# Optimization experiments

Hardware: AMD Instinct MI355X
Metric: run time of the kernel (lower is better)

Reference implementation:

```python
import jax, jax.numpy as jnp
import numpy as np

EMB = 1024
HEADS = 16
HEAD_DIM = EMB // HEADS


def setup_inputs() -> dict:
    key = jax.random.key(0)
    ks = jax.random.split(key, 6)
    B, S = 4, 1024
    inputs = jax.random.normal(ks[0], (B, S, EMB), dtype=jnp.float32)
    # causal mask: 1.0 where attention is disallowed (added * -1e9 in the layer)
    mask = (1.0 - jnp.tril(jnp.ones((S, S), dtype=jnp.float32)))[None, None, :, :]
    scale = 1.0 / np.sqrt(EMB)
    wq = jax.random.normal(ks[1], (EMB, EMB), dtype=jnp.float32) * scale
    wk = jax.random.normal(ks[2], (EMB, EMB), dtype=jnp.float32) * scale
    wv = jax.random.normal(ks[3], (EMB, EMB), dtype=jnp.float32) * scale
    wo = jax.random.normal(ks[4], (EMB, EMB), dtype=jnp.float32) * scale
    zb = jnp.zeros((EMB,), dtype=jnp.float32)
    return {"inputs": inputs, "mask": mask, "wq": wq, "bq": zb, "wk": wk,
            "bk": zb, "wv": wv, "bv": zb, "wo": wo, "bo": zb}


def _split_heads(t, B):
    # [B, S, E] -> [B, H, S, Dh]
    return t.reshape(B, -1, HEADS, HEAD_DIM).transpose(0, 2, 1, 3)


def reference(inputs, mask, wq, bq, wk, bk, wv, bv, wo, bo):
    B = inputs.shape[0]
    q = _split_heads(inputs @ wq + bq, B)
    k = _split_heads(inputs @ wk + bk, B)
    v = _split_heads(inputs @ wv + bv, B)
    # NOTE: source divides by sqrt(sqrt(head_num)) = head_num**0.25
    scores = jnp.einsum('bhsd,bhtd->bhst', q, k) / jnp.asarray(HEADS, inputs.dtype) ** 0.25
    if mask is not None:
        scores = scores + mask * -1e9
    attn = jax.nn.softmax(scores, axis=-1)
    z = jnp.einsum('bhst,bhtd->bhsd', attn, v)
    # Faithful to source: reshape [B,H,S,Dh] -> [B,S,E] WITHOUT transposing heads back
    z = z.reshape(B, -1, EMB)
    return z @ wo + bo
```

## Files before the change

kernel.cpp:

```cpp
#include <hip/hip_runtime.h>
#include <hip/hip_bf16.h>
#include <stdint.h>

typedef __attribute__((ext_vector_type(8))) short short8;
typedef __attribute__((ext_vector_type(4))) float float4v;

#define SEQ   1024
#define NQKV  3072

__device__ __forceinline__ float bf2f(ushort h) {
    union { uint u; float f; } c; c.u = ((uint)h) << 16; return c.f;
}
__device__ __forceinline__ ushort f2bf(float f) {
    union { uint u; float f; } c; c.f = f;
    uint u = c.u;
    return (ushort)((u + 0x7fffu + ((u >> 16) & 1u)) >> 16);
}
__device__ __forceinline__ void gl2lds16(const ushort* g, ushort* l) {
    __builtin_amdgcn_global_load_lds(
        (const __attribute__((address_space(1))) unsigned int*)(g),
        (__attribute__((address_space(3))) unsigned int*)(l),
        16, 0, 0);
}

__global__ void detect_k(const uint* __restrict__ x, int* __restrict__ flag) {
    __shared__ int cnt[256];
    int h = 0;
    for (int i = threadIdx.x; i < 4096; i += 256) {
        uint w = x[i];
        uint e = (w >> 7) & 0xFFu;
        h += (e >= 100u && e <= 130u) ? 1 : 0;
    }
    cnt[threadIdx.x] = h;
    __syncthreads();
    if (threadIdx.x == 0) {
        int s = 0;
        for (int i = 0; i < 256; i++) s += cnt[i];
        flag[0] = (s > 2048) ? 0 : 1;
    }
}

__global__ __launch_bounds__(256) void xcvt_k(const void* __restrict__ x,
                                              ushort* __restrict__ xc,
                                              const int* __restrict__ flag) {
    if (!*flag) return;
    int i = (blockIdx.x * 256 + threadIdx.x) * 4;
    const float* xf = (const float*)x;
    float4 v = *(const float4*)(xf + i);
    ushort4 o;
    o.x = f2bf(v.x); o.y = f2bf(v.y); o.z = f2bf(v.z); o.w = f2bf(v.w);
    *(ushort4*)(xc + i) = o;
}

__global__ void biascat_k(const void* __restrict__ bq, const void* __restrict__ bk,
                          const void* __restrict__ bv, const void* __restrict__ bo,
                          const int* __restrict__ flag, ushort* __restrict__ bout) {
    int i = blockIdx.x * 256 + threadIdx.x;
    int sel = i >> 10, j = i & 1023;
    const void* p = (sel == 0) ? bq : (sel == 1) ? bk : (sel == 2) ? bv : bo;
    bout[i] = (*flag) ? f2bf(((const float*)p)[j]) : ((const ushort*)p)[j];
}

__global__ __launch_bounds__(256) void transpose4_k(const void* __restrict__ w0,
                                                    const void* __restrict__ w1,
                                                    const void* __restrict__ w2,
                                                    const void* __restrict__ w3,
                                                    ushort* __restrict__ outall,
                                                    const int* __restrict__ flag) {
    __shared__ ushort tile[64][72];
    int z = blockIdx.z;
    const void* in = (z == 0) ? w0 : (z == 1) ? w1 : (z == 2) ? w2 : w3;
    ushort* out = outall + (size_t)z * 1024 * 1024;
    int k0 = blockIdx.x * 64;
    int n0 = blockIdx.y * 64;
    int t = threadIdx.x;
    int r = t >> 3, c = (t & 7) * 8;
    bool isf = (*flag != 0);
#pragma unroll
    for (int p = 0; p < 2; p++) {
        int rr = r + p * 32;
        if (isf) {
            const float* src = (const float*)in + (size_t)(k0 + rr) * 1024 + n0 + c;
            float4 v0 = *(const float4*)src;
            float4 v1 = *(const float4*)(src + 4);
            tile[rr][c + 0] = f2bf(v0.x); tile[rr][c + 1] = f2bf(v0.y);
            tile[rr][c + 2] = f2bf(v0.z); tile[rr][c + 3] = f2bf(v0.w);
            tile[rr][c + 4] = f2bf(v1.x); tile[rr][c + 5] = f2bf(v1.y);
            tile[rr][c + 6] = f2bf(v1.z); tile[rr][c + 7] = f2bf(v1.w);
        } else {
            uint4 v = *(const uint4*)((const ushort*)in + (size_t)(k0 + rr) * 1024 + n0 + c);
            *(uint4*)&tile[rr][c] = v;
        }
    }
    __syncthreads();
#pragma unroll
    for (int p = 0; p < 2; p++) {
        int n = r + p * 32;
        ushort vals[8];
#pragma unroll
        for (int j = 0; j < 8; j++) vals[j] = tile[c + j][n];
        *(uint4*)(out + (size_t)(n0 + n) * 1024 + k0 + c) = *(uint4*)vals;
    }
}

template <bool VOUT, bool DUAL>
__global__ __launch_bounds__(256) void gemm128_k(const ushort* __restrict__ Araw,
                                                 const ushort* __restrict__ Aconv,
                                                 const ushort* __restrict__ BT,
                                                 const ushort* __restrict__ bias,
                                                 void* __restrict__ C,
                                                 ushort* __restrict__ vtout,
                                                 const int* __restrict__ flag,
                                                 int M, int N, int K) {
    __shared__ ushort As[128 * 32];
    __shared__ ushort Bs[128 * 32];
    int n0 = blockIdx.x * 128, m0 = blockIdx.y * 128;
    int t = threadIdx.x;
    int w = t >> 6, lane = t & 63, q = lane >> 4, ln = lane & 15;
    int wr = w >> 1, wc = w & 1;
    const ushort* A = (*flag) ? Aconv : Araw;

    float4v acc[4][4];
#pragma unroll
    for (int r = 0; r < 4; r++)
#pragma unroll
        for (int cc = 0; cc < 4; cc++) acc[r][cc] = (float4v){0.f, 0.f, 0.f, 0.f};

    for (int k0 = 0; k0 < K; k0 += 32) {
#pragma unroll
        for (int j = 0; j < 2; j++) {
            int c = j * 256 + t;
            int row = c >> 2, s = c & 3;
            int kc = s ^ ((row >> 1) & 3);
            gl2lds16(A + (size_t)(m0 + row) * K + k0 + kc * 8, &As[c * 8]);
            gl2lds16(BT + (size_t)(n0 + row) * K + k0 + kc * 8, &Bs[c * 8]);
        }
        __syncthreads();
        short8 af[4], bf[4];
#pragma unroll
        for (int r = 0; r < 4; r++) {
            int row = wr * 64 + r * 16 + ln;
            af[r] = *(const short8*)&As[((row << 2) | (q ^ ((row >> 1) & 3))) * 8];
            int col = wc * 64 + r * 16 + ln;
            bf[r] = *(const short8*)&Bs[((col << 2) | (q ^ ((col >> 1) & 3))) * 8];
        }
#pragma unroll
        for (int r = 0; r < 4; r++)
#pragma unroll
            for (int cc = 0; cc < 4; cc++)
                acc[r][cc] = __builtin_amdgcn_mfma_f32_16x16x32_bf16(af[r], bf[cc], acc[r][cc], 0, 0, 0);
        __syncthreads();
    }

    if (VOUT && n0 >= 2048) {
#pragma unroll
        for (int cc = 0; cc < 4; cc++) {
            int n = n0 + wc * 64 + cc * 16 + ln;
            int hd = n - 2048, hh = hd >> 6, dd = hd & 63;
            float bs = bf2f(bias[n]);
#pragma unroll
            for (int r = 0; r < 4; r++) {
                int mb = m0 + wr * 64 + r * 16 + q * 4;
                int b = mb >> 10, srow = mb & 1023;
                ushort4 o4;
                o4.x = f2bf(acc[r][cc][0] + bs);
                o4.y = f2bf(acc[r][cc][1] + bs);
                o4.z = f2bf(acc[r][cc][2] + bs);
                o4.w = f2bf(acc[r][cc][3] + bs);
                *(ushort4*)(vtout + ((size_t)(b * 16 + hh) * 64 + dd) * 1024 + srow) = o4;
            }
        }
        return;
    }
    bool outf = DUAL && (*flag != 0);
#pragma unroll
    for (int cc = 0; cc < 4; cc++) {
        int n = n0 + wc * 64 + cc * 16 + ln;
        float bs = bf2f(bias[n]);
#pragma unroll
        for (int r = 0; r < 4; r++) {
#pragma unroll
            for (int i = 0; i < 4; i++) {
                int m = m0 + wr * 64 + r * 16 + q * 4 + i;
                float v = acc[r][cc][i] + bs;
                if (outf) ((float*)C)[(size_t)m * N + n] = v;
                else      ((ushort*)C)[(size_t)m * N + n] = f2bf(v);
            }
        }
    }
}

__global__ __launch_bounds__(256) void attn_k(const ushort* __restrict__ qkv,
                                              const ushort* __restrict__ vt,
                                              ushort* __restrict__ zp) {
    __shared__ ushort Ks[2][64 * 64];
    __shared__ ushort Vs[2][64 * 64];
    __shared__ ushort PA[4][16 * 76];
    __shared__ ushort PB[4][16 * 76];
    int pr = blockIdx.x;
    int bh = blockIdx.y;
    int b = bh >> 4, h = bh & 15;
    int t = threadIdx.x;
    int w = t >> 6, lane = t & 63, q = lane >> 4, ln = lane & 15;

    const float CE = 0.72134752f;

    const ushort* Qp = qkv + (size_t)(b * SEQ) * NQKV + h * 64;
    const ushort* Kp = qkv + (size_t)(b * SEQ) * NQKV + 1024 + h * 64;
    const ushort* Vt = vt + (size_t)bh * 64 * 1024;

    int c0 = t, c1 = 256 + t;
    int row0 = c0 >> 3, kc0 = (c0 & 7) ^ (row0 & 7);
    int row1 = c1 >> 3, kc1 = (c1 & 7) ^ (row1 & 7);

    int tiA = pr, tiB = 15 - pr;
    int swA = tiA * 64 + w * 16, swB = tiB * 64 + w * 16;

    short8 aqA0 = *(const short8*)(Qp + (size_t)(swA + ln) * NQKV + q * 8);
    short8 aqA1 = *(const short8*)(Qp + (size_t)(swA + ln) * NQKV + 32 + q * 8);
    short8 aqB0 = *(const short8*)(Qp + (size_t)(swB + ln) * NQKV + q * 8);
    short8 aqB1 = *(const short8*)(Qp + (size_t)(swB + ln) * NQKV + 32 + q * 8);

    float lA[4], lB[4];
    float4v oA[4], oB[4];
#pragma unroll
    for (int i = 0; i < 4; i++) { lA[i] = 0.f; lB[i] = 0.f; }
#pragma unroll
    for (int nb = 0; nb < 4; nb++) {
        oA[nb] = (float4v){0.f, 0.f, 0.f, 0.f};
        oB[nb] = (float4v){0.f, 0.f, 0.f, 0.f};
    }

    gl2lds16(Kp + (size_t)row0 * NQKV + kc0 * 8, &Ks[0][c0 * 8]);
    gl2lds16(Vt + (size_t)row0 * 1024 + kc0 * 8, &Vs[0][c0 * 8]);
    gl2lds16(Kp + (size_t)row1 * NQKV + kc1 * 8, &Ks[0][c1 * 8]);
    gl2lds16(Vt + (size_t)row1 * 1024 + kc1 * 8, &Vs[0][c1 * 8]);

    auto tile_step = [&](int cur, int t0, int sw, short8 aq0, short8 aq1,
                         float* lp, float4v* o, ushort* Pw, bool maskdiag) {
        float4v s[4];
#pragma unroll
        for (int nb = 0; nb < 4; nb++) {
            int row = nb * 16 + ln;
            short8 kf0 = *(const short8*)&Ks[cur][((row << 3) | (q ^ (row & 7))) * 8];
            short8 kf1 = *(const short8*)&Ks[cur][((row << 3) | ((4 + q) ^ (row & 7))) * 8];
            s[nb] = (float4v){0.f, 0.f, 0.f, 0.f};
            s[nb] = __builtin_amdgcn_mfma_f32_16x16x32_bf16(aq0, kf0, s[nb], 0, 0, 0);
            s[nb] = __builtin_amdgcn_mfma_f32_16x16x32_bf16(aq1, kf1, s[nb], 0, 0, 0);
        }
        float p[4][4];
        if (!maskdiag) {
#pragma unroll
            for (int nb = 0; nb < 4; nb++)
#pragma unroll
                for (int i = 0; i < 4; i++) p[nb][i] = exp2f(s[nb][i] * CE);
        } else {
#pragma unroll
            for (int nb = 0; nb < 4; nb++)
#pragma unroll
                for (int i = 0; i < 4; i++) {
                    int srow = sw + q * 4 + i;
                    int col = t0 + nb * 16 + ln;
                    p[nb][i] = exp2f((col <= srow) ? s[nb][i] * CE : -1e30f);
                }
        }
#pragma unroll
        for (int i = 0; i < 4; i++)
            lp[i] += (p[0][i] + p[1][i]) + (p[2][i] + p[3][i]);
#pragma unroll
        for (int nb = 0; nb < 4; nb++)
#pragma unroll
            for (int i = 0; i < 4; i++)
                Pw[(q * 4 + i) * 76 + nb * 16 + ln] = f2bf(p[nb][i]);
        asm volatile("s_waitcnt lgkmcnt(0)\n" ::: "memory");
        short8 ap0 = *(const short8*)&Pw[ln * 76 + q * 8];
        short8 ap1 = *(const short8*)&Pw[ln * 76 + 32 + q * 8];
#pragma unroll
        for (int nb = 0; nb < 4; nb++) {
            int row = nb * 16 + ln;
            short8 bv0 = *(const short8*)&Vs[cur][((row << 3) | (q ^ (row & 7))) * 8];
            short8 bv1 = *(const short8*)&Vs[cur][((row << 3) | ((4 + q) ^ (row & 7))) * 8];
            o[nb] = __builtin_amdgcn_mfma_f32_16x16x32_bf16(ap0, bv0, o[nb], 0, 0, 0);
            o[nb] = __builtin_amdgcn_mfma_f32_16x16x32_bf16(ap1, bv1, o[nb], 0, 0, 0);
        }
    };

    for (int kt = 0; kt <= tiB; kt++) {
        int cur = kt & 1;
        int t0 = kt * 64;
        __syncthreads();
        if (kt < tiB) {
            int nt0 = t0 + 64, nxt = cur ^ 1;
            gl2lds16(Kp + (size_t)(nt0 + row0) * NQKV + kc0 * 8, &Ks[nxt][c0 * 8]);
            gl2lds16(Vt + (size_t)row0 * 1024 + nt0 + kc0 * 8, &Vs[nxt][c0 * 8]);
            gl2lds16(Kp + (size_t)(nt0 + row1) * NQKV + kc1 * 8, &Ks[nxt][c1 * 8]);
            gl2lds16(Vt + (size_t)row1 * 1024 + nt0 + kc1 * 8, &Vs[nxt][c1 * 8]);
        }
        tile_step(cur, t0, swB, aqB0, aqB1, lB, oB, PB[w], kt == tiB);
        if (kt <= tiA)
            tile_step(cur, t0, swA, aqA0, aqA1, lA, oA, PA[w], kt == tiA);
    }

#pragma unroll
    for (int i = 0; i < 4; i++) {
        float sA = lA[i], sB = lB[i];
#pragma unroll
        for (int mk = 1; mk < 16; mk <<= 1) {
            sA += __shfl_xor(sA, mk, 64);
            sB += __shfl_xor(sB, mk, 64);
        }
        lA[i] = sA; lB[i] = sB;
    }
#pragma unroll
    for (int nb = 0; nb < 4; nb++) {
#pragma unroll
        for (int i = 0; i < 4; i++) {
            int d = nb * 16 + ln;
            int srowA = swA + q * 4 + i;
            int spA = h * 64 + (srowA >> 4);
            int epA = ((srowA & 15) << 6) + d;
            zp[((size_t)(b * SEQ + spA)) * 1024 + epA] = f2bf(oA[nb][i] / lA[i]);
            int srowB = swB + q * 4 + i;
            int spB = h * 64 + (srowB >> 4);
            int epB = ((srowB & 15) << 6) + d;
            zp[((size_t)(b * SEQ + spB)) * 1024 + epB] = f2bf(oB[nb][i] / lB[i]);
        }
    }
}

extern "C" void kernel_launch(void* const* d_in, const int* in_sizes, int n_in,
                              void* d_out, int out_size, void* d_ws, size_t ws_size,
                              hipStream_t stream) {
    const void* X  = d_in[0];
    const void* wq = d_in[2];
    const void* bq = d_in[3];
    const void* wk = d_in[4];
    const void* bk = d_in[5];
    const void* wv = d_in[6];
    const void* bv = d_in[7];
    const void* wo = d_in[8];
    const void* bo = d_in[9];

    char* ws = (char*)d_ws;
    int*    flag  = (int*)ws;
    ushort* biasq = (ushort*)(ws + 4096);
    ushort* WTall = (ushort*)(ws + 12288);
    ushort* Xc    = (ushort*)(ws + 8400896);
    ushort* QKV   = (ushort*)(ws + 16789504);
    ushort* VT    = (ushort*)(ws + 41955328);
    ushort* WTo   = WTall + 3 * 1024 * 1024;
    ushort* ZP    = Xc;

    detect_k<<<1, 256, 0, stream>>>((const uint*)X, flag);
    xcvt_k<<<4096, 256, 0, stream>>>(X, Xc, flag);
    biascat_k<<<16, 256, 0, stream>>>(bq, bk, bv, bo, flag, biasq);
    transpose4_k<<<dim3(16, 16, 4), 256, 0, stream>>>(wq, wk, wv, wo, WTall, flag);
    gemm128_k<true, false><<<dim3(24, 32), 256, 0, stream>>>(
        (const ushort*)X, Xc, WTall, biasq, QKV, VT, flag, 4096, NQKV, 1024);
    attn_k<<<dim3(8, 64), 256, 0, stream>>>(QKV, VT, ZP);
    gemm128_k<false, true><<<dim3(8, 32), 256, 0, stream>>>(
        ZP, ZP, WTo, biasq + 3072, d_out, nullptr, flag, 4096, 1024, 1024);
}
```

Measured before the change: 219.8 us.

## Split V transpose into separate kernel and use 64-row tiles for output GEMM

The QKV GEMM no longer writes V transposed from its epilogue, which used scattered ushort4 stores. A dedicated LDS-tiled transpose kernel now builds VT from the QKV buffer with coalesced writes. The GEMM is templated on the M tile, and the output projection uses BM=64, doubling its block count from 256 to 512 so more CUs have work. The cost is one extra kernel launch and an extra read and write of V.

```diff
diff --git a/kernel.cpp b/kernel.cpp
--- a/kernel.cpp
+++ b/kernel.cpp
@@ -103,85 +103,99 @@
     }
 }
 
-template <bool VOUT, bool DUAL>
-__global__ __launch_bounds__(256) void gemm128_k(const ushort* __restrict__ Araw,
-                                                 const ushort* __restrict__ Aconv,
-                                                 const ushort* __restrict__ BT,
-                                                 const ushort* __restrict__ bias,
-                                                 void* __restrict__ C,
-                                                 ushort* __restrict__ vtout,
-                                                 const int* __restrict__ flag,
-                                                 int M, int N, int K) {
-    __shared__ ushort As[128 * 32];
+__global__ __launch_bounds__(256) void vtrans_k(const ushort* __restrict__ qkv,
+                                                ushort* __restrict__ vt) {
+    __shared__ ushort tile[64][72];
+    int t0 = blockIdx.x * 64;
+    int bh = blockIdx.y;
+    int b = bh >> 4, h = bh & 15;
+    int t = threadIdx.x;
+    int r = t >> 3, c = (t & 7) * 8;
+#pragma unroll
+    for (int p = 0; p < 2; p++) {
+        int rr = r + p * 32;
+        uint4 v = *(const uint4*)(qkv + (size_t)(b * 1024 + t0 + rr) * NQKV + 2048 + h * 64 + c);
+        *(uint4*)&tile[rr][c] = v;
+    }
+    __syncthreads();
+#pragma unroll
+    for (int p = 0; p < 2; p++) {
+        int d = r + p * 32;
+        ushort vals[8];
+#pragma unroll
+        for (int j = 0; j < 8; j++) vals[j] = tile[c + j][d];
+        *(uint4*)(vt + ((size_t)bh * 64 + d) * 1024 + t0 + c) = *(uint4*)vals;
+    }
+}
+
+template <int BM, bool DUAL>
+__global__ __launch_bounds__(256) void gemm_k(const ushort* __restrict__ Araw,
+                                              const ushort* __restrict__ Aconv,
+                                              const ushort* __restrict__ BT,
+                                              const ushort* __restrict__ bias,
+                                              void* __restrict__ C,
+                                              const int* __restrict__ flag,
+                                              int M, int N, int K) {
+    constexpr int RM = BM / 32;
+    __shared__ ushort As[BM * 32];
     __shared__ ushort Bs[128 * 32];
-    int n0 = blockIdx.x * 128, m0 = blockIdx.y * 128;
+    int n0 = blockIdx.x * 128, m0 = blockIdx.y * BM;
     int t = threadIdx.x;
     int w = t >> 6, lane = t & 63, q = lane >> 4, ln = lane & 15;
     int wr = w >> 1, wc = w & 1;
     const ushort* A = (*flag) ? Aconv : Araw;
 
-    float4v acc[4][4];
-#pragma unroll
-    for (int r = 0; r < 4; r++)
+    float4v acc[RM][4];
+#pragma unroll
+    for (int r = 0; r < RM; r++)
 #pragma unroll
         for (int cc = 0; cc < 4; cc++) acc[r][cc] = (float4v){0.f, 0.f, 0.f, 0.f};
 
     for (int k0 = 0; k0 < K; k0 += 32) {
+#pragma unroll
+        for (int j = 0; j < BM / 64; j++) {
+            int c = j * 256 + t;
+            int row = c >> 2, s = c & 3;
+            int kc = s ^ ((row >> 1) & 3);
+            gl2lds16(A + (size_t)(m0 + row) * K + k0 + kc * 8, &As[c * 8]);
+        }
 #pragma unroll
         for (int j = 0; j < 2; j++) {
             int c = j * 256 + t;
             int row = c >> 2, s = c & 3;
             int kc = s ^ ((row >> 1) & 3);
-            gl2lds16(A + (size_t)(m0 + row) * K + k0 + kc * 8, &As[c * 8]);
             gl2lds16(BT + (size_t)(n0 + row) * K + k0 + kc * 8, &Bs[c * 8]);
         }
         __syncthreads();
-        short8 af[4], bf[4];
-#pragma unroll
-        for (int r = 0; r < 4; r++) {
-            int row = wr * 64 + r * 16 + ln;
+        short8 af[RM], bf[4];
+#pragma unroll
+        for (int r = 0; r < RM; r++) {
+            int row = wr * (BM / 2) + r * 16 + ln;
             af[r] = *(const short8*)&As[((row << 2) | (q ^ ((row >> 1) & 3))) * 8];
-            int col = wc * 64 + r * 16 + ln;
-            bf[r] = *(const short8*)&Bs[((col << 2) | (q ^ ((col >> 1) & 3))) * 8];
-        }
-#pragma unroll
-        for (int r = 0; r < 4; r++)
+        }
+#pragma unroll
+        for (int cc = 0; cc < 4; cc++) {
+            int col = wc * 64 + cc * 16 + ln;
+            bf[cc] = *(const short8*)&Bs[((col << 2) | (q ^ ((col >> 1) & 3))) * 8];
+        }
+#pragma unroll
+        for (int r = 0; r < RM; r++)
 #pragma unroll
             for (int cc = 0; cc < 4; cc++)
                 acc[r][cc] = __builtin_amdgcn_mfma_f32_16x16x32_bf16(af[r], bf[cc], acc[r][cc], 0, 0, 0);
         __syncthreads();
     }
 
-    if (VOUT && n0 >= 2048) {
-#pragma unroll
-        for (int cc = 0; cc < 4; cc++) {
-            int n = n0 + wc * 64 + cc * 16 + ln;
-            int hd = n - 2048, hh = hd >> 6, dd = hd & 63;
-            float bs = bf2f(bias[n]);
-#pragma unroll
-            for (int r = 0; r < 4; r++) {
-                int mb = m0 + wr * 64 + r * 16 + q * 4;
-                int b = mb >> 10, srow = mb & 1023;
-                ushort4 o4;
-                o4.x = f2bf(acc[r][cc][0] + bs);
-                o4.y = f2bf(acc[r][cc][1] + bs);
-                o4.z = f2bf(acc[r][cc][2] + bs);
-                o4.w = f2bf(acc[r][cc][3] + bs);
-                *(ushort4*)(vtout + ((size_t)(b * 16 + hh) * 64 + dd) * 1024 + srow) = o4;
-            }
-        }
-        return;
-    }
     bool outf = DUAL && (*flag != 0);
 #pragma unroll
     for (int cc = 0; cc < 4; cc++) {
         int n = n0 + wc * 64 + cc * 16 + ln;
         float bs = bf2f(bias[n]);
 #pragma unroll
-        for (int r = 0; r < 4; r++) {
+        for (int r = 0; r < RM; r++) {
 #pragma unroll
             for (int i = 0; i < 4; i++) {
-                int m = m0 + wr * 64 + r * 16 + q * 4 + i;
+                int m = m0 + wr * (BM / 2) + r * 16 + q * 4 + i;
                 float v = acc[r][cc][i] + bs;
                 if (outf) ((float*)C)[(size_t)m * N + n] = v;
                 else      ((ushort*)C)[(size_t)m * N + n] = f2bf(v);
@@ -355,9 +369,10 @@
     xcvt_k<<<4096, 256, 0, stream>>>(X, Xc, flag);
     biascat_k<<<16, 256, 0, stream>>>(bq, bk, bv, bo, flag, biasq);
     transpose4_k<<<dim3(16, 16, 4), 256, 0, stream>>>(wq, wk, wv, wo, WTall, flag);
-    gemm128_k<true, false><<<dim3(24, 32), 256, 0, stream>>>(
-        (const ushort*)X, Xc, WTall, biasq, QKV, VT, flag, 4096, NQKV, 1024);
+    gemm_k<128, false><<<dim3(24, 32), 256, 0, stream>>>(
+        (const ushort*)X, Xc, WTall, biasq, QKV, flag, 4096, NQKV, 1024);
+    vtrans_k<<<dim3(16, 64), 256, 0, stream>>>(QKV, VT);
     attn_k<<<dim3(8, 64), 256, 0, stream>>>(QKV, VT, ZP);
-    gemm128_k<false, true><<<dim3(8, 32), 256, 0, stream>>>(
-        ZP, ZP, WTo, biasq + 3072, d_out, nullptr, flag, 4096, 1024, 1024);
-}
+    gemm_k<64, true><<<dim3(8, 64), 256, 0, stream>>>(
+        ZP, ZP, WTo, biasq + 3072, d_out, flag, 4096, 1024, 1024);
+}
```

New measurement: 202.0 us. 1.09x faster.
